# Kernel tuning notes

Measured on AMD Instinct MI355X. Metric: run time of the kernel, lower is better.

Reference implementation:

```python
import jax, jax.numpy as jnp
import numpy as np

B, L, Q = 1024, 200, 1
DQ, DF = 512, 128
H, D1, D2 = 4, 128, 64


def setup_inputs() -> dict:
    key = jax.random.key(0)
    ks = jax.random.split(key, 20)
    inp = {
        "query": jax.random.normal(ks[0], (B, Q, DQ), jnp.float32),
        "fact": jax.random.normal(ks[1], (B, L, DF), jnp.float32),
        "mask": jax.random.randint(ks[2], (B, L), 0, 2, jnp.int32),
        "mm_cosine": jax.random.normal(ks[3], (2, B, L), jnp.float32),
    }
    # per-head FCRepeat weights, init per reset_parameters: randn/sqrt(fan_in), bias 0.1
    def w(k, fan_in, fan_out):
        return jax.random.normal(k, (H, fan_in, fan_out), jnp.float32) / np.sqrt(fan_in).astype(np.float32)
    inp["Wq1"] = w(ks[4], DQ, D1); inp["bq1"] = jnp.full((H, D1), 0.1, jnp.float32)
    inp["Wq2"] = w(ks[5], D1, D2); inp["bq2"] = jnp.full((H, D2), 0.1, jnp.float32)
    inp["Wf1"] = w(ks[6], DF, D1); inp["bf1"] = jnp.full((H, D1), 0.1, jnp.float32)
    inp["Wf2"] = w(ks[7], D1, D2); inp["bf2"] = jnp.full((H, D2), 0.1, jnp.float32)
    inp["Wv1"] = w(ks[8], DF, D1); inp["bv1"] = jnp.full((H, D1), 0.1, jnp.float32)
    inp["Wv2"] = w(ks[9], D1, D2); inp["bv2"] = jnp.full((H, D2), 0.1, jnp.float32)
    inp["tau1"] = jnp.full((2, H), 0.1, jnp.float32)   # cosine_tau1
    inp["tau2"] = jnp.full((3, H), 1.0, jnp.float32)   # cosine_tau2
    return inp


def _silu(x):
    return x * jax.nn.sigmoid(x)


def reference(query, fact, mask, mm_cosine,
              Wq1, bq1, Wq2, bq2, Wf1, bf1, Wf2, bf2, Wv1, bv1, Wv2, bv2,
              tau1, tau2):
    # per-head FC stacks (identity acts inside FCRepeat), then SiLU gating
    fq = jnp.einsum('bqi,hio->hbqo', query, Wq1) + bq1[:, None, None, :]
    fq = jnp.einsum('hbqi,hio->hbqo', fq, Wq2) + bq2[:, None, None, :]
    fq = _silu(fq)                                   # [H,B,1,D2]
    ff = jnp.einsum('bli,hio->hblo', fact, Wf1) + bf1[:, None, None, :]
    ff = jnp.einsum('hbli,hio->hblo', ff, Wf2) + bf2[:, None, None, :]
    ff = _silu(ff)                                   # [H,B,L,D2]
    fv = jnp.einsum('bli,hio->hblo', fact, Wv1) + bv1[:, None, None, :]
    fv = jnp.einsum('hbli,hio->hblo', fv, Wv2) + bv2[:, None, None, :]
    fv = _silu(fv)                                   # [H,B,L,D2]

    dot = jnp.einsum('hbld,hbqd->hblq', ff, fq)      # [H,B,L,1]
    dot = dot + (-1e9) * (1.0 - mask.astype(jnp.float32))[None, :, :, None]

    # cosine-bias cross terms
    bias = (mm_cosine[0][None] / tau1[0][:, None, None]
            + mm_cosine[1][None] / tau1[1][:, None, None])[..., None]  # [H,B,L,1]
    b1, b2, b3 = (tau2[i][:, None, None, None] for i in range(3))
    dot = b1 * dot + b2 * bias + b3 * dot * bias

    alphas = jax.nn.softmax(dot, axis=2) + 1e-7      # softmax over L
    out = jnp.einsum('hbld,hblq->hbdq', fv, alphas)[..., 0]  # [H,B,D2]
    return jnp.transpose(out, (1, 0, 2)).reshape(out.shape[1], -1)  # [B,H*D2]
```

## Files before the change

### kernel.cpp

```cpp
#include <hip/hip_runtime.h>
#include <hip/hip_bf16.h>

typedef __attribute__((ext_vector_type(8))) short short8;
typedef __attribute__((ext_vector_type(4))) float f32x4;

#define NH   4
#define NB   1024
#define NL   200
#define NDQ  512
#define NDF  128
#define ND1  128
#define ND2  64
#define KP   128
#define NW   13
#define NT   (NW*64)
#define SGRAN (3*ND2*16)

#define OFF_WQC   0
#define OFF_BQC   (NH*NDQ*ND2*4)
#define OFF_FQ    (OFF_BQC + NH*ND2*4)
#define OFF_WIMG  (OFF_FQ + NH*NB*ND2*4)
#define OFF_BFC   (OFF_WIMG + NH*3*ND2*KP*2)
#define OFF_BVC   (OFF_BFC + NH*ND2*4)

__device__ inline short f2bf(float f) {
    union { float f; unsigned u; } v; v.f = f;
    unsigned r = (v.u + 0x7FFFu + ((v.u >> 16) & 1u)) >> 16;
    return (short)r;
}
__device__ inline float bf2f(short s) {
    union { unsigned u; float f; } v; v.u = ((unsigned)(unsigned short)s) << 16;
    return v.f;
}
__device__ inline float fsilu(float z) {
    return z * __fdividef(1.f, 1.f + __expf(-z));
}

__global__ __launch_bounds__(256) void k_combine(
    const float* __restrict__ Wq1, const float* __restrict__ bq1,
    const float* __restrict__ Wq2, const float* __restrict__ bq2,
    const float* __restrict__ Wf1, const float* __restrict__ bf1,
    const float* __restrict__ Wf2, const float* __restrict__ bf2,
    const float* __restrict__ Wv1, const float* __restrict__ bv1,
    const float* __restrict__ Wv2, const float* __restrict__ bv2,
    float* __restrict__ WQC, float* __restrict__ BQC,
    __hip_bfloat16* __restrict__ WIMG, float* __restrict__ BFC, float* __restrict__ BVC)
{
    int g = blockIdx.x * 256 + threadIdx.x;
    if (g < NH*NDQ*ND2) {
        int h = g >> 15, r = g & 32767, i = r >> 6, j = r & 63;
        const float* a  = Wq1 + (h*NDQ + i)*ND1;
        const float* bb = Wq2 + h*ND1*ND2 + j;
        float s = 0.f;
        for (int k = 0; k < ND1; ++k) s += a[k] * bb[k*ND2];
        WQC[(h*NDQ + i)*ND2 + j] = s;
        return;
    }
    g -= NH*NDQ*ND2;
    if (g < 2*NH*NDF*ND2) {
        int which = (g >= NH*NDF*ND2);
        int r0 = g & (NH*NDF*ND2 - 1);
        int h = r0 >> 13, r = r0 & 8191, i = r >> 6, j = r & 63;
        const float* W1 = (which ? Wv1 : Wf1) + (h*NDF + i)*ND1;
        const float* W2 = (which ? Wv2 : Wf2) + h*ND1*ND2 + j;
        float s = 0.f;
        for (int k = 0; k < ND1; ++k) s += W1[k] * W2[k*ND2];
        short hi = f2bf(s);
        short lo = f2bf(s - bf2f(hi));
        __hip_bfloat16* img = WIMG + (size_t)((h*3 + (which ? 2 : 0))*ND2 + j)*KP + i;
        ((short*)img)[0] = hi;
        if (!which) ((short*)img)[ND2*KP] = lo;
        return;
    }
    g -= 2*NH*NDF*ND2;
    if (g < NH*ND2) {
        int h = g >> 6, j = g & 63;
        float s = bq2[h*ND2 + j];
        for (int k = 0; k < ND1; ++k) s += bq1[h*ND1 + k] * Wq2[(h*ND1 + k)*ND2 + j];
        BQC[g] = s; return;
    }
    g -= NH*ND2;
    if (g < NH*ND2) {
        int h = g >> 6, j = g & 63;
        float s = bf2[h*ND2 + j];
        for (int k = 0; k < ND1; ++k) s += bf1[h*ND1 + k] * Wf2[(h*ND1 + k)*ND2 + j];
        BFC[g] = s; return;
    }
    g -= NH*ND2;
    if (g < NH*ND2) {
        int h = g >> 6, j = g & 63;
        float s = bv2[h*ND2 + j];
        for (int k = 0; k < ND1; ++k) s += bv1[h*ND1 + k] * Wv2[(h*ND1 + k)*ND2 + j];
        BVC[g] = s; return;
    }
}

__global__ __launch_bounds__(256) void k_fq(
    const float* __restrict__ query, const float* __restrict__ WQC,
    const float* __restrict__ BQC, float* __restrict__ FQ)
{
    __shared__ __align__(16) float qS[2*NDQ];
    const int t = threadIdx.x;
    const int b0 = blockIdx.x * 2;
    {
        const float4* src = (const float4*)(query + (size_t)b0 * NDQ);
        ((float4*)qS)[t] = src[t];
    }
    __syncthreads();
    const int h = t >> 6, d = t & 63;
    float s0, s1;
    s0 = s1 = BQC[h*ND2 + d];
    const float* wp = WQC + (size_t)h*NDQ*ND2 + d;
    #pragma unroll 16
    for (int i = 0; i < NDQ; ++i) {
        float wv = wp[i*ND2];
        s0 += qS[i]       * wv;
        s1 += qS[NDQ + i] * wv;
    }
    float* o = FQ + ((size_t)h*NB + b0)*ND2 + d;
    o[0]   = fsilu(s0);
    o[ND2] = fsilu(s1);
}

__global__ __launch_bounds__(NT) void k_main(
    const float* __restrict__ fact,
    const int* __restrict__ mask,
    const float* __restrict__ mmc,
    const float* __restrict__ tau1,
    const float* __restrict__ tau2,
    const float* __restrict__ FQ,
    const float* __restrict__ BFC,
    const float* __restrict__ BVC,
    const __hip_bfloat16* __restrict__ WIMG,
    float* __restrict__ out)
{
    __shared__ __align__(16) __hip_bfloat16 wS[2][3*ND2*KP];
    __shared__ __align__(16) float pS[2][NW][132];
    __shared__ __align__(16) float fqS[NH][ND2];
    __shared__ __align__(16) float bfcS[NH][ND2];
    __shared__ __align__(16) float bvcS[NH][ND2];

    const int t    = threadIdx.x;
    const int b    = blockIdx.x;
    const int w    = t >> 6;
    const int lane = t & 63;
    const int a15  = lane & 15;
    const int quad = lane >> 4;
    const int qrot = quad + 2*(a15 & 7);

    const int bL = b * NL;

    float4 sreg[4];
    {
        const float4* src = (const float4*)WIMG;
        #pragma unroll
        for (int k = 0; k < 4; ++k) { int i = t + k*NT; if (i < SGRAN) sreg[k] = src[i]; }
    }
    float cval = 0.f;
    if (t < 256)       cval = FQ[(((size_t)(t >> 6))*NB + b)*ND2 + (t & 63)];
    else if (t < 512)  cval = BFC[t - 256];
    else if (t < 768)  cval = BVC[t - 512];
    float mkv[4], c0v[4], c1v[4];
    {
        int rbase = w*16 + quad*4;
        for (int rg = 0; rg < 4; ++rg) {
            int r = rbase + rg;
            if (r < NL) {
                mkv[rg] = 1e9f * (1.0f - (float)mask[bL + r]);
                c0v[rg] = mmc[bL + r];
                c1v[rg] = mmc[NB*NL + bL + r];
            } else { mkv[rg] = 0.f; c0v[rg] = 0.f; c1v[rg] = 0.f; }
        }
    }

    short8 afh[4], afl[4];
    const short8 zero8 = {0,0,0,0,0,0,0,0};
    {
        int row = w*16 + a15;
        for (int kk = 0; kk < 4; ++kk) {
            short8 vh = zero8, vl = zero8;
            if (row < NL) {
                const float* p = fact + ((size_t)(bL + row))*NDF + kk*32 + quad*8;
                float4 x0 = *(const float4*)p;
                float4 x1 = *(const float4*)(p + 4);
                float v[8] = {x0.x, x0.y, x0.z, x0.w, x1.x, x1.y, x1.z, x1.w};
                for (int j = 0; j < 8; ++j) {
                    short hs = f2bf(v[j]);
                    vh[j] = hs;
                    vl[j] = f2bf(v[j] - bf2f(hs));
                }
            }
            afh[kk] = vh;
            afl[kk] = vl;
        }
    }

    {
        float4* dst = (float4*)&wS[0][0];
        #pragma unroll
        for (int k = 0; k < 4; ++k) {
            int i = t + k*NT;
            if (i < SGRAN) {
                int row = i >> 4, g = i & 15;
                dst[row*16 + ((g + 2*(row & 7)) & 15)] = sreg[k];
            }
        }
    }
    if (t < 256)       ((float*)fqS)[t]        = cval;
    else if (t < 512)  ((float*)bfcS)[t - 256] = cval;
    else if (t < 768)  ((float*)bvcS)[t - 512] = cval;
    __syncthreads();

    const f32x4 zf = {0.f, 0.f, 0.f, 0.f};

    for (int h = 0; h < NH; ++h) {
        if (h + 1 < NH) {
            const float4* src = (const float4*)(WIMG + (size_t)((h+1)*3)*ND2*KP);
            #pragma unroll
            for (int k = 0; k < 4; ++k) { int i = t + k*NT; if (i < SGRAN) sreg[k] = src[i]; }
        }
        if (h > 0 && w == 8 + h) {
            const int ps = (h - 1) & 1;
            float M = pS[ps][0][0];
            for (int ww = 1; ww < NW; ++ww) M = fmaxf(M, pS[ps][ww][0]);
            float den = 0.f, num = 0.f, s1 = 0.f;
            for (int ww = 0; ww < NW; ++ww) {
                float e = __expf(pS[ps][ww][0] - M);
                den += e * pS[ps][ww][1];
                num += e * pS[ps][ww][2 + lane];
                s1  += pS[ps][ww][66 + lane];
            }
            out[(size_t)b*(NH*ND2) + (h-1)*ND2 + lane] = num * __fdividef(1.f, den) + 1e-7f * s1;
        }

        const float rt1a = __fdividef(1.f, tau1[h]);
        const float rt1b = __fdividef(1.f, tau1[NH + h]);
        const float t20 = tau2[h];
        const float t21 = tau2[NH + h];
        const float t22 = tau2[2*NH + h];

        float fqv[4], bfcv[4];
        for (int nt = 0; nt < 4; ++nt) {
            fqv[nt]  = fqS[h][nt*16 + a15];
            bfcv[nt] = bfcS[h][nt*16 + a15];
        }

        const __hip_bfloat16* wb = &wS[h & 1][0];

        f32x4 acc[4];
        for (int nt = 0; nt < 4; ++nt) acc[nt] = zf;
        __builtin_amdgcn_s_setprio(1);
        for (int kk = 0; kk < 4; ++kk) {
            const int gk = ((kk*4 + qrot) & 15) << 3;
            short8 bh[4], bl[4];
            for (int nt = 0; nt < 4; ++nt) {
                const __hip_bfloat16* p = wb + (nt*16 + a15)*KP + gk;
                bh[nt] = *(const short8*)p;
                bl[nt] = *(const short8*)(p + ND2*KP);
            }
            for (int nt = 0; nt < 4; ++nt) {
                acc[nt] = __builtin_amdgcn_mfma_f32_16x16x32_bf16(afh[kk], bh[nt], acc[nt], 0, 0, 0);
                acc[nt] = __builtin_amdgcn_mfma_f32_16x16x32_bf16(afh[kk], bl[nt], acc[nt], 0, 0, 0);
                acc[nt] = __builtin_amdgcn_mfma_f32_16x16x32_bf16(afl[kk], bh[nt], acc[nt], 0, 0, 0);
            }
        }
        __builtin_amdgcn_s_setprio(0);

        float lg[4];
        for (int rg = 0; rg < 4; ++rg) {
            float l = -3.0e38f;
            float s = 0.f;
            for (int nt = 0; nt < 4; ++nt)
                s += fsilu(acc[nt][rg] + bfcv[nt]) * fqv[nt];
            s += __shfl_xor(s, 1);
            s += __shfl_xor(s, 2);
            s += __shfl_xor(s, 4);
            s += __shfl_xor(s, 8);
            int r = w*16 + quad*4 + rg;
            if (r < NL) {
                float dv = s - mkv[rg];
                float bias = c0v[rg]*rt1a + c1v[rg]*rt1b;
                l = t20*dv + t21*bias + t22*dv*bias;
            }
            lg[rg] = l;
        }

        float m = fmaxf(fmaxf(lg[0], lg[1]), fmaxf(lg[2], lg[3]));
        m = fmaxf(m, __shfl_xor(m, 16));
        m = fmaxf(m, __shfl_xor(m, 32));
        float sw = 0.f;
        for (int rg = 0; rg < 4; ++rg) {
            float p = __expf(lg[rg] - m);
            lg[rg] = p;
            sw += p;
        }
        sw += __shfl_xor(sw, 16);
        sw += __shfl_xor(sw, 32);

        for (int nt = 0; nt < 4; ++nt) acc[nt] = zf;
        __builtin_amdgcn_s_setprio(1);
        for (int kk = 0; kk < 4; ++kk) {
            const int gk = ((kk*4 + qrot) & 15) << 3;
            short8 bv[4];
            for (int nt = 0; nt < 4; ++nt)
                bv[nt] = *(const short8*)(wb + (2*ND2 + nt*16 + a15)*KP + gk);
            for (int nt = 0; nt < 4; ++nt)
                acc[nt] = __builtin_amdgcn_mfma_f32_16x16x32_bf16(afh[kk], bv[nt], acc[nt], 0, 0, 0);
        }
        __builtin_amdgcn_s_setprio(0);

        float bvcv[4];
        for (int nt = 0; nt < 4; ++nt) bvcv[nt] = bvcS[h][nt*16 + a15];
        float oE[4] = {0.f,0.f,0.f,0.f}, oS[4] = {0.f,0.f,0.f,0.f};
        for (int rg = 0; rg < 4; ++rg) {
            float p = lg[rg];
            int r = w*16 + quad*4 + rg;
            float vm = (r < NL) ? 1.f : 0.f;
            for (int nt = 0; nt < 4; ++nt) {
                float sv = fsilu(acc[nt][rg] + bvcv[nt]);
                oE[nt] += p * sv;
                oS[nt] += vm * sv;
            }
        }
        for (int nt = 0; nt < 4; ++nt) {
            oE[nt] += __shfl_xor(oE[nt], 16);
            oE[nt] += __shfl_xor(oE[nt], 32);
            oS[nt] += __shfl_xor(oS[nt], 16);
            oS[nt] += __shfl_xor(oS[nt], 32);
        }
        if (lane == 0) { pS[h & 1][w][0] = m; pS[h & 1][w][1] = sw; }
        if (quad == 0)
            for (int nt = 0; nt < 4; ++nt) {
                pS[h & 1][w][2  + nt*16 + a15] = oE[nt];
                pS[h & 1][w][66 + nt*16 + a15] = oS[nt];
            }

        if (h + 1 < NH) {
            float4* dst = (float4*)&wS[(h+1) & 1][0];
            #pragma unroll
            for (int k = 0; k < 4; ++k) {
                int i = t + k*NT;
                if (i < SGRAN) {
                    int row = i >> 4, g = i & 15;
                    dst[row*16 + ((g + 2*(row & 7)) & 15)] = sreg[k];
                }
            }
        }
        __syncthreads();
    }

    if (w == 12) {
        const int ps = (NH - 1) & 1;
        float M = pS[ps][0][0];
        for (int ww = 1; ww < NW; ++ww) M = fmaxf(M, pS[ps][ww][0]);
        float den = 0.f, num = 0.f, s1 = 0.f;
        for (int ww = 0; ww < NW; ++ww) {
            float e = __expf(pS[ps][ww][0] - M);
            den += e * pS[ps][ww][1];
            num += e * pS[ps][ww][2 + lane];
            s1  += pS[ps][ww][66 + lane];
        }
        out[(size_t)b*(NH*ND2) + (NH-1)*ND2 + lane] = num * __fdividef(1.f, den) + 1e-7f * s1;
    }
}

extern "C" void kernel_launch(void* const* d_in, const int* in_sizes, int n_in,
                              void* d_out, int out_size, void* d_ws, size_t ws_size,
                              hipStream_t stream) {
    const float* query = (const float*)d_in[0];
    const float* fact  = (const float*)d_in[1];
    const int*   maskp = (const int*)d_in[2];
    const float* mmc   = (const float*)d_in[3];
    const float* Wq1 = (const float*)d_in[4];
    const float* bq1 = (const float*)d_in[5];
    const float* Wq2 = (const float*)d_in[6];
    const float* bq2 = (const float*)d_in[7];
    const float* Wf1 = (const float*)d_in[8];
    const float* bf1 = (const float*)d_in[9];
    const float* Wf2 = (const float*)d_in[10];
    const float* bf2 = (const float*)d_in[11];
    const float* Wv1 = (const float*)d_in[12];
    const float* bv1 = (const float*)d_in[13];
    const float* Wv2 = (const float*)d_in[14];
    const float* bv2 = (const float*)d_in[15];
    const float* tau1 = (const float*)d_in[16];
    const float* tau2 = (const float*)d_in[17];

    char* ws = (char*)d_ws;
    float*          WQC  = (float*)(ws + OFF_WQC);
    float*          BQC  = (float*)(ws + OFF_BQC);
    float*          FQ   = (float*)(ws + OFF_FQ);
    __hip_bfloat16* WIMG = (__hip_bfloat16*)(ws + OFF_WIMG);
    float*          BFC  = (float*)(ws + OFF_BFC);
    float*          BVC  = (float*)(ws + OFF_BVC);

    k_combine<<<771, 256, 0, stream>>>(Wq1, bq1, Wq2, bq2, Wf1, bf1, Wf2, bf2,
                                       Wv1, bv1, Wv2, bv2, WQC, BQC, WIMG, BFC, BVC);
    k_fq<<<NB/2, 256, 0, stream>>>(query, WQC, BQC, FQ);
    k_main<<<NB, NT, 0, stream>>>(fact, maskp, mmc, tau1, tau2, FQ, BFC, BVC, WIMG,
                                  (float*)d_out);
}
```

Before: 361.6 us.

## Stream per-head weight images directly into LDS with global_load_lds

The per-head bf16 weight image is no longer staged through registers and then written to shared memory. It is now copied straight into the double-buffered LDS slot with 16-byte global_load_lds instructions, and the swizzle is moved to the global source offsets. This removes the register pressure and the LDS store instructions of the manual copy, and lets the copy run alongside the head's compute. The launch bounds now also ask for 4 blocks per CU, which could force a tight register budget and cause spills.

```diff
diff --git a/kernel.cpp b/kernel.cpp
--- a/kernel.cpp
+++ b/kernel.cpp
@@ -14,14 +14,19 @@
 #define KP   128
 #define NW   13
 #define NT   (NW*64)
+#define HIMG (3*ND2*KP*2)
 #define SGRAN (3*ND2*16)
 
 #define OFF_WQC   0
 #define OFF_BQC   (NH*NDQ*ND2*4)
 #define OFF_FQ    (OFF_BQC + NH*ND2*4)
 #define OFF_WIMG  (OFF_FQ + NH*NB*ND2*4)
-#define OFF_BFC   (OFF_WIMG + NH*3*ND2*KP*2)
+#define OFF_BFC   (OFF_WIMG + NH*HIMG)
 #define OFF_BVC   (OFF_BFC + NH*ND2*4)
+
+#define GLOAD_LDS16(gp, lp) __builtin_amdgcn_global_load_lds(                 \
+    (const __attribute__((address_space(1))) void*)(gp),                      \
+    (__attribute__((address_space(3))) void*)(lp), 16, 0, 0)
 
 __device__ inline short f2bf(float f) {
     union { float f; unsigned u; } v; v.f = f;
@@ -122,7 +127,7 @@
     o[ND2] = fsilu(s1);
 }
 
-__global__ __launch_bounds__(NT) void k_main(
+__global__ __launch_bounds__(NT, 4) void k_main(
     const float* __restrict__ fact,
     const int* __restrict__ mask,
     const float* __restrict__ mmc,
@@ -150,12 +155,23 @@
 
     const int bL = b * NL;
 
-    float4 sreg[4];
-    {
-        const float4* src = (const float4*)WIMG;
-        #pragma unroll
-        for (int k = 0; k < 4; ++k) { int i = t + k*NT; if (i < SGRAN) sreg[k] = src[i]; }
-    }
+    int srcOff[4], ldsByte[4];
+    bool cOk[4];
+    #pragma unroll
+    for (int j = 0; j < 4; ++j) {
+        int c = w*4 + j;
+        cOk[j] = (c < SGRAN/64);
+        int i = c*64 + lane;
+        int row = i >> 4, gp = i & 15;
+        int g = (gp - 2*(row & 7)) & 15;
+        srcOff[j] = (row*16 + g) * 16;
+        ldsByte[j] = c * 1024;
+    }
+    #pragma unroll
+    for (int j = 0; j < 4; ++j)
+        if (cOk[j])
+            GLOAD_LDS16((const char*)WIMG + srcOff[j], (char*)&wS[0][0] + ldsByte[j]);
+
     float cval = 0.f;
     if (t < 256)       cval = FQ[(((size_t)(t >> 6))*NB + b)*ND2 + (t & 63)];
     else if (t < 512)  cval = BFC[t - 256];
@@ -195,17 +211,6 @@
         }
     }
 
-    {
-        float4* dst = (float4*)&wS[0][0];
-        #pragma unroll
-        for (int k = 0; k < 4; ++k) {
-            int i = t + k*NT;
-            if (i < SGRAN) {
-                int row = i >> 4, g = i & 15;
-                dst[row*16 + ((g + 2*(row & 7)) & 15)] = sreg[k];
-            }
-        }
-    }
     if (t < 256)       ((float*)fqS)[t]        = cval;
     else if (t < 512)  ((float*)bfcS)[t - 256] = cval;
     else if (t < 768)  ((float*)bvcS)[t - 512] = cval;
@@ -215,9 +220,11 @@
 
     for (int h = 0; h < NH; ++h) {
         if (h + 1 < NH) {
-            const float4* src = (const float4*)(WIMG + (size_t)((h+1)*3)*ND2*KP);
+            const char* hb = (const char*)WIMG + (size_t)(h+1)*HIMG;
+            char* lb = (char*)&wS[(h+1) & 1][0];
             #pragma unroll
-            for (int k = 0; k < 4; ++k) { int i = t + k*NT; if (i < SGRAN) sreg[k] = src[i]; }
+            for (int j = 0; j < 4; ++j)
+                if (cOk[j]) GLOAD_LDS16(hb + srcOff[j], lb + ldsByte[j]);
         }
         if (h > 0 && w == 8 + h) {
             const int ps = (h - 1) & 1;
@@ -334,18 +341,6 @@
                 pS[h & 1][w][2  + nt*16 + a15] = oE[nt];
                 pS[h & 1][w][66 + nt*16 + a15] = oS[nt];
             }
-
-        if (h + 1 < NH) {
-            float4* dst = (float4*)&wS[(h+1) & 1][0];
-            #pragma unroll
-            for (int k = 0; k < 4; ++k) {
-                int i = t + k*NT;
-                if (i < SGRAN) {
-                    int row = i >> 4, g = i & 15;
-                    dst[row*16 + ((g + 2*(row & 7)) & 15)] = sreg[k];
-                }
-            }
-        }
         __syncthreads();
     }
 
```

Result: faster. 344.3 us (-4.8%).
